# Kernel optimization log

Measured on AMD Instinct MI355X. Metric: run time of the kernel, lower is better.

## Reference

```python
import jax, jax.numpy as jnp
import numpy as np
from jax import lax

B, N, G, K, D = 16, 8192, 256, 64, 256
DEPTH, H, HID, PH = 4, 8, 1024, 128
EPS = 1e-5
BN_SCALE = float(1.0 / np.sqrt(1.0 + 1e-5))  # BatchNorm eval, running mean 0 / var 1


def setup_inputs() -> dict:
    key = jax.random.key(0)
    ks = iter(jax.random.split(key, 48))
    def rn(shape, s=0.02):
        return jax.random.normal(next(ks), shape, jnp.float32) * s
    z = lambda *s: jnp.zeros(s, jnp.float32)
    o = lambda *s: jnp.ones(s, jnp.float32)
    return dict(
        x=jax.random.normal(next(ks), (B, N, 3), jnp.float32),
        enc_w1=rn((3, 128)), enc_b1=z(128), enc_bn1_g=o(128), enc_bn1_b=z(128),
        enc_w2=rn((128, 256)), enc_b2=z(256),
        enc_w3=rn((512, 512)), enc_b3=z(512), enc_bn2_g=o(512), enc_bn2_b=z(512),
        enc_w4=rn((512, D)), enc_b4=z(D),
        cls_token=rn((1, 1, D)), cls_pos=rn((1, 1, D)),
        pos_w1=rn((3, 128)), pos_b1=z(128), pos_w2=rn((128, D)), pos_b2=z(D),
        ln1_g=o(DEPTH, D), ln1_b=z(DEPTH, D),
        qkv_w=rn((DEPTH, D, 3 * D)),
        proj_w=rn((DEPTH, D, D)), proj_b=z(DEPTH, D),
        ln2_g=o(DEPTH, D), ln2_b=z(DEPTH, D),
        fc1_w=rn((DEPTH, D, HID)), fc1_b=z(DEPTH, HID),
        fc2_w=rn((DEPTH, HID, D)), fc2_b=z(DEPTH, D),
        norm_g=o(D), norm_b=z(D),
        head_w1=rn((D + 3, PH)), head_b1=z(PH), head_w2=rn((PH, 1)), head_b2=z(1),
    )


def layernorm(t, g, b):
    m = jnp.mean(t, -1, keepdims=True)
    v = jnp.mean((t - m) ** 2, -1, keepdims=True)
    return (t - m) / jnp.sqrt(v + EPS) * g + b


def fps(xyz, num_group):
    # farthest point sampling; deterministic start at index 0 (torch uses randint)
    Bb, Nn, _ = xyz.shape
    def body(i, st):
        dist, far, idxs = st
        idxs = idxs.at[:, i].set(far)
        cen = jnp.take_along_axis(xyz, far[:, None, None], axis=1)  # (B,1,3)
        d = jnp.sum((xyz - cen) ** 2, -1)
        dist = jnp.minimum(dist, d)
        far = jnp.argmax(dist, axis=1).astype(jnp.int32)
        return (dist, far, idxs)
    st0 = (jnp.full((Bb, Nn), 1e10, jnp.float32),
           jnp.zeros((Bb,), jnp.int32),
           jnp.zeros((Bb, num_group), jnp.int32))
    _, _, idxs = lax.fori_loop(0, num_group, body, st0)
    centers = jnp.take_along_axis(xyz, idxs[..., None], axis=1)  # (B,G,3)
    return centers, idxs


def knn(xyz, centers, k):
    # squared-distance cdist (same argsort order as p=2) + topk smallest
    c2 = jnp.sum(centers ** 2, -1)[:, :, None]
    x2 = jnp.sum(xyz ** 2, -1)[:, None, :]
    d2 = c2 + x2 - 2.0 * jnp.einsum('bgd,bnd->bgn', centers, xyz)  # (B,G,N)
    idx = lax.top_k(-d2, k)[1]  # (B,G,k)
    neigh = jax.vmap(lambda p, i: p[i])(xyz, idx)  # (B,G,k,3)
    return idx, neigh


def _forward(x, enc_w1, enc_b1, enc_bn1_g, enc_bn1_b, enc_w2, enc_b2,
             enc_w3, enc_b3, enc_bn2_g, enc_bn2_b, enc_w4, enc_b4,
             cls_token, cls_pos, pos_w1, pos_b1, pos_w2, pos_b2,
             ln1_g, ln1_b, qkv_w, proj_w, proj_b, ln2_g, ln2_b,
             fc1_w, fc1_b, fc2_w, fc2_b, norm_g, norm_b,
             head_w1, head_b1, head_w2, head_b2):
    Bb, Nn, _ = x.shape
    # grouping is @torch.no_grad() in the original -> stop_gradient
    pts = lax.stop_gradient(x)
    centers, _ = fps(pts, G)
    idx, neigh = knn(pts, centers, K)
    neigh = neigh - centers[:, :, None, :]  # (B,G,K,3) centered

    # PointNet encoder (kernel-size-1 convs == matmuls; BN eval with unit stats)
    pg = neigh.reshape(Bb * G, K, 3)
    h = pg @ enc_w1 + enc_b1                                # (BG,K,128)
    h = jax.nn.relu(h * enc_bn1_g * BN_SCALE + enc_bn1_b)
    h = h @ enc_w2 + enc_b2                                 # (BG,K,256)
    gmax = jnp.max(h, axis=1, keepdims=True)                # (BG,1,256)
    h = jnp.concatenate([jnp.broadcast_to(gmax, h.shape), h], -1)  # (BG,K,512)
    h = h @ enc_w3 + enc_b3
    h = jax.nn.relu(h * enc_bn2_g * BN_SCALE + enc_bn2_b)
    h = h @ enc_w4 + enc_b4                                 # (BG,K,D)
    tokens = jnp.max(h, axis=1).reshape(Bb, G, D)

    pos = jax.nn.gelu(centers @ pos_w1 + pos_b1, approximate=False) @ pos_w2 + pos_b2
    xt = jnp.concatenate([jnp.broadcast_to(cls_token, (Bb, 1, D)), tokens], 1)
    pt = jnp.concatenate([jnp.broadcast_to(cls_pos, (Bb, 1, D)), pos], 1)

    scale = (D // H) ** -0.5
    for l in range(DEPTH):
        xi = xt + pt  # pos added before every block
        h1 = layernorm(xi, ln1_g[l], ln1_b[l])
        qkv = (h1 @ qkv_w[l]).reshape(Bb, G + 1, 3, H, D // H).transpose(2, 0, 3, 1, 4)
        q, k_, v = qkv[0], qkv[1], qkv[2]
        attn = jax.nn.softmax(jnp.einsum('bhnd,bhmd->bhnm', q, k_) * scale, -1)
        o = jnp.einsum('bhnm,bhmd->bhnd', attn, v).transpose(0, 2, 1, 3).reshape(Bb, G + 1, D)
        xi = xi + o @ proj_w[l] + proj_b[l]
        h2 = layernorm(xi, ln2_g[l], ln2_b[l])
        xi = xi + jax.nn.gelu(h2 @ fc1_w[l] + fc1_b[l], approximate=False) @ fc2_w[l] + fc2_b[l]
        xt = xi
    xt = layernorm(xt, norm_g, norm_b)

    gfeat = xt[:, 1:, :]  # (B,G,D)
    concat = jnp.concatenate(
        [jnp.broadcast_to(gfeat[:, :, None, :], (Bb, G, K, D)), neigh], -1)  # (B,G,K,D+3)
    lg = (jax.nn.relu(concat @ head_w1 + head_b1) @ head_w2 + head_b2)[..., 0]  # (B,G,K)

    # scatter-mean per-point logits over original N points
    flat_i = idx.reshape(Bb, G * K)
    flat_v = lg.reshape(Bb, G * K)
    sums = jax.vmap(lambda v, i: jax.ops.segment_sum(v, i, num_segments=N))(flat_v, flat_i)
    cnts = jax.vmap(lambda i: jax.ops.segment_sum(jnp.ones(i.shape, jnp.float32), i, num_segments=N))(flat_i)
    return sums / jnp.maximum(cnts, 1.0)  # (B,N)


def reference(x, enc_w1, enc_b1, enc_bn1_g, enc_bn1_b, enc_w2, enc_b2,
              enc_w3, enc_b3, enc_bn2_g, enc_bn2_b, enc_w4, enc_b4,
              cls_token, cls_pos, pos_w1, pos_b1, pos_w2, pos_b2,
              ln1_g, ln1_b, qkv_w, proj_w, proj_b, ln2_g, ln2_b,
              fc1_w, fc1_b, fc2_w, fc2_b, norm_g, norm_b,
              head_w1, head_b1, head_w2, head_b2):
    return _forward(x, enc_w1, enc_b1, enc_bn1_g, enc_bn1_b, enc_w2, enc_b2,
                    enc_w3, enc_b3, enc_bn2_g, enc_bn2_b, enc_w4, enc_b4,
                    cls_token, cls_pos, pos_w1, pos_b1, pos_w2, pos_b2,
                    ln1_g, ln1_b, qkv_w, proj_w, proj_b, ln2_g, ln2_b,
                    fc1_w, fc1_b, fc2_w, fc2_b, norm_g, norm_b,
                    head_w1, head_b1, head_w2, head_b2)
```

## Files before the change

kernel.cpp:

```cpp
#include <hip/hip_runtime.h>
#include <hip/hip_bf16.h>

#define B_ 16
#define N_ 8192
#define G_ 256
#define K_ 64
#define D_ 256
#define HID_ 1024
#define EPS_ 1e-5f

typedef __attribute__((ext_vector_type(8))) short bf16x8;
typedef __attribute__((ext_vector_type(4))) float f32x4;

__device__ __forceinline__ float bf16_to_f32(unsigned short u){
  unsigned int v = ((unsigned int)u) << 16;
  return __uint_as_float(v);
}
__device__ __forceinline__ unsigned short f32_to_bf16(float f){
  unsigned int u = __float_as_uint(f);
  unsigned int r = (u + 0x7FFFu + ((u >> 16) & 1u)) >> 16;
  return (unsigned short)r;
}
__device__ __forceinline__ unsigned short bf16h(float a){
  __hip_bfloat16 h = __float2bfloat16(a);
  union { __hip_bfloat16 h; unsigned short u; } cv; cv.h = h; return cv.u;
}
__device__ __forceinline__ float gelu_exact(float v){
  return 0.5f * v * (1.0f + erff(v * 0.70710678118654752440f));
}

template<int CTRL>
__device__ __forceinline__ unsigned long long dpp64(unsigned long long k){
  int lo = (int)(unsigned int)k;
  int hi = (int)(unsigned int)(k >> 32);
  int dlo = __builtin_amdgcn_update_dpp(lo, lo, CTRL, 0xF, 0xF, false);
  int dhi = __builtin_amdgcn_update_dpp(hi, hi, CTRL, 0xF, 0xF, false);
  return (((unsigned long long)(unsigned int)dhi) << 32) | (unsigned int)dlo;
}
__device__ __forceinline__ unsigned long long bcast64(unsigned long long k, int lane){
  unsigned int lo = (unsigned int)__builtin_amdgcn_readlane((int)(unsigned int)k, lane);
  unsigned int hi = (unsigned int)__builtin_amdgcn_readlane((int)(unsigned int)(k >> 32), lane);
  return (((unsigned long long)hi) << 32) | lo;
}
__device__ __forceinline__ unsigned long long wave_max64(unsigned long long k){
  unsigned long long t;
  t = dpp64<0x111>(k); if (t > k) k = t;
  t = dpp64<0x112>(k); if (t > k) k = t;
  t = dpp64<0x114>(k); if (t > k) k = t;
  t = dpp64<0x118>(k); if (t > k) k = t;
  t = dpp64<0x142>(k); if (t > k) k = t;
  t = dpp64<0x143>(k); if (t > k) k = t;
  return bcast64(k, 63);
}
__device__ __forceinline__ unsigned long long wave_min64(unsigned long long k){
  unsigned long long t;
  t = dpp64<0x111>(k); if (t < k) k = t;
  t = dpp64<0x112>(k); if (t < k) k = t;
  t = dpp64<0x114>(k); if (t < k) k = t;
  t = dpp64<0x118>(k); if (t < k) k = t;
  t = dpp64<0x142>(k); if (t < k) k = t;
  t = dpp64<0x143>(k); if (t < k) k = t;
  return bcast64(k, 63);
}
__device__ __forceinline__ unsigned long long red8_max64(unsigned long long k){
  unsigned long long t;
  t = dpp64<0x111>(k); if (t > k) k = t;
  t = dpp64<0x112>(k); if (t > k) k = t;
  t = dpp64<0x114>(k); if (t > k) k = t;
  return bcast64(k, 7);
}
__device__ __forceinline__ unsigned long long red4_min64(unsigned long long k){
  unsigned long long t;
  t = dpp64<0x111>(k); if (t < k) k = t;
  t = dpp64<0x112>(k); if (t < k) k = t;
  return bcast64(k, 3);
}

__device__ __forceinline__ void packHi(const float* __restrict__ W, unsigned short* __restrict__ hi,
                                       int f, int N, int ksBits){
  int j = f & 7, lane = (f >> 3) & 63;
  int ks = (f >> 9) & ((1 << ksBits) - 1);
  int nt = f >> (9 + ksBits);
  int k = ks * 32 + ((lane >> 4) & 3) * 8 + j, c = nt * 16 + (lane & 15);
  hi[f] = f32_to_bf16(W[(size_t)k * N + c]);
}

__global__ __launch_bounds__(512) void prep_fps_kernel(
    const float* __restrict__ x, float* __restrict__ centers,
    const float* __restrict__ w1, const float* __restrict__ b1,
    const float* __restrict__ g1, const float* __restrict__ bb1,
    const float* __restrict__ w3, const float* __restrict__ b3,
    const float* __restrict__ g2, const float* __restrict__ bb2,
    const float* __restrict__ enc_w2, const float* __restrict__ enc_w4,
    const float* __restrict__ qkv_w, const float* __restrict__ proj_w,
    const float* __restrict__ fc1_w, const float* __restrict__ fc2_w,
    float* __restrict__ w1f, float* __restrict__ b1f, float* __restrict__ b3f,
    unsigned short* __restrict__ w2ph, unsigned short* __restrict__ w2pl,
    unsigned short* __restrict__ w3ph, unsigned short* __restrict__ w4ph,
    unsigned short* __restrict__ qkvPh, unsigned short* __restrict__ projPh,
    unsigned short* __restrict__ fc1Ph, unsigned short* __restrict__ fc2Ph,
    unsigned short* __restrict__ w3tp)
{
  const float S = 0.99999500003749968f;
  int blk = blockIdx.x, tid = threadIdx.x;

  if (blk >= 17){
    int f = (blk - 17) * 512 + tid;
    if (f < 32768){
      int j = f & 7, lane = (f >> 3) & 63, ks = (f >> 9) & 3, nt = f >> 11;
      int k = ks * 32 + ((lane >> 4) & 3) * 8 + j, c = nt * 16 + (lane & 15);
      float v = enc_w2[(size_t)k * 256 + c];
      unsigned short h = f32_to_bf16(v);
      w2ph[f] = h; w2pl[f] = f32_to_bf16(v - bf16_to_f32(h));
    } else if (f < 163840){
      f -= 32768;
      int j = f & 7, lane = (f >> 3) & 63, ks = (f >> 9) & 7, nt = f >> 12;
      int k = ks * 32 + ((lane >> 4) & 3) * 8 + j, c = nt * 16 + (lane & 15);
      w3ph[f] = f32_to_bf16(w3[(size_t)(256 + k) * 512 + c] * g2[c] * S);
    } else if (f < 294912){
      f -= 163840;
      packHi(enc_w4, w4ph, f, 256, 4);
    } else if (f < 1081344){
      f -= 294912;
      int l = f / 196608, fl = f - l * 196608;
      packHi(qkv_w + (size_t)l * 196608, qkvPh + (size_t)l * 196608, fl, 768, 3);
    } else if (f < 1343488){
      f -= 1081344;
      int l = f >> 16, fl = f & 65535;
      packHi(proj_w + (size_t)l * 65536, projPh + (size_t)l * 65536, fl, 256, 3);
    } else if (f < 2392064){
      f -= 1343488;
      int l = f >> 18, fl = f & 262143;
      packHi(fc1_w + (size_t)l * 262144, fc1Ph + (size_t)l * 262144, fl, 1024, 3);
    } else if (f < 3440640){
      f -= 2392064;
      int l = f >> 18, fl = f & 262143;
      packHi(fc2_w + (size_t)l * 262144, fc2Ph + (size_t)l * 262144, fl, 256, 5);
    } else {
      f -= 3440640;
      int j = f & 7, lane = (f >> 3) & 63, ks = (f >> 9) & 7, nt = f >> 12;
      int k = ks * 32 + ((lane >> 4) & 3) * 8 + j, c = nt * 16 + (lane & 15);
      w3tp[f] = f32_to_bf16(w3[(size_t)k * 512 + c] * g2[c] * S);
    }
    return;
  }
  if (blk == 16){
    if (tid < 384) w1f[tid] = w1[tid] * g1[tid & 127] * S;
    if (tid < 128) b1f[tid] = b1[tid] * g1[tid] * S + bb1[tid];
    b3f[tid] = b3[tid] * g2[tid] * S + bb2[tid];
    return;
  }

  int b = blk;
  const float* xb = x + (size_t)b * N_ * 3;
  int lane = tid & 63, wave = tid >> 6;
  float px[16], py[16], pz[16], dist[16];
#pragma unroll
  for (int j = 0; j < 16; j++){
    int p = tid + j * 512;
    px[j] = xb[p*3+0]; py[j] = xb[p*3+1]; pz[j] = xb[p*3+2];
    dist[j] = 1e10f;
  }
  __shared__ unsigned long long slotK[2][8];
  __shared__ float4 slotC[2][8];
  __shared__ float sCen[G_ * 3];
  float cx = xb[0], cy = xb[1], cz = xb[2];
  for (int i = 0; i < G_; i++){
    if (tid == 0){
      sCen[i*3+0] = cx; sCen[i*3+1] = cy; sCen[i*3+2] = cz;
    }
    float bestv = -1.0f; int bestj = 0;
#pragma unroll
    for (int j = 0; j < 16; j++){
      float dx = __fadd_rn(px[j], -cx);
      float dy = __fadd_rn(py[j], -cy);
      float dz = __fadd_rn(pz[j], -cz);
      float d  = __fadd_rn(__fadd_rn(__fmul_rn(dx,dx), __fmul_rn(dy,dy)), __fmul_rn(dz,dz));
      float dm = fminf(dist[j], d);
      dist[j] = dm;
      if (dm > bestv){ bestv = dm; bestj = j; }
    }
    unsigned int pid = (unsigned int)(tid + bestj * 512);
    unsigned long long key = (((unsigned long long)__float_as_uint(bestv)) << 32) | (unsigned long long)(~pid);
    key = wave_max64(key);
    int par = i & 1;
    unsigned int wpid = ~(unsigned int)key;
    if (lane == (int)(wpid & 63)){
      int jj = (int)(wpid >> 9);
      float fx = px[0], fy = py[0], fz = pz[0];
#pragma unroll
      for (int j = 1; j < 16; j++) if (jj == j){ fx = px[j]; fy = py[j]; fz = pz[j]; }
      slotK[par][wave] = key;
      slotC[par][wave] = make_float4(fx, fy, fz, 0.0f);
    }
    __syncthreads();
    if (i + 1 < G_){
      int sl = lane & 7;
      unsigned long long k2 = slotK[par][sl];
      float4 cc4 = slotC[par][sl];
      k2 = red8_max64(k2);
      unsigned int gpid = ~(unsigned int)k2;
      int s = (int)((gpid & 511u) >> 6);
      cx = __uint_as_float((unsigned int)__builtin_amdgcn_readlane((int)__float_as_uint(cc4.x), s));
      cy = __uint_as_float((unsigned int)__builtin_amdgcn_readlane((int)__float_as_uint(cc4.y), s));
      cz = __uint_as_float((unsigned int)__builtin_amdgcn_readlane((int)__float_as_uint(cc4.z), s));
    }
  }
  __syncthreads();
  for (int e = tid; e < G_ * 3; e += 512)
    centers[(size_t)b * G_ * 3 + e] = sCen[e];
}

__global__ __launch_bounds__(256) void knn_kernel(const float* __restrict__ x, const float* __restrict__ centers,
                                                  int* __restrict__ knn_idx, float* __restrict__ neigh)
{
  int blk = blockIdx.x, b = blk >> 8;
  const float* xb = x + (size_t)b * N_ * 3;
  const float* cc = centers + (size_t)blk * 3;
  int tid = threadIdx.x, lane = tid & 63, wave = tid >> 6;
  float c0 = cc[0], c1 = cc[1], c2v = cc[2];
  float c2s = __fadd_rn(__fadd_rn(__fmul_rn(c0,c0), __fmul_rn(c1,c1)), __fmul_rn(c2v,c2v));
  float d[32];
#pragma unroll
  for (int j = 0; j < 32; j++){
    int p = tid + j * 256;
    float x0 = xb[p*3+0], x1 = xb[p*3+1], x2 = xb[p*3+2];
    float xs = __fadd_rn(__fadd_rn(__fmul_rn(x0,x0), __fmul_rn(x1,x1)), __fmul_rn(x2,x2));
    float dt = __fadd_rn(__fadd_rn(__fmul_rn(c0,x0), __fmul_rn(c1,x1)), __fmul_rn(c2v,x2));
    d[j] = __fadd_rn(__fadd_rn(c2s, xs), -__fmul_rn(2.0f, dt));
  }
  const float FINF = __int_as_float(0x7F800000);
  float lmin = FINF; unsigned int lp = 0xFFFFFFFFu;
#pragma unroll
  for (int j = 0; j < 32; j++){ if (d[j] < lmin){ lmin = d[j]; lp = (unsigned int)(tid + j*256); } }
  __shared__ unsigned long long wred[2][4];
  __shared__ int sIdx[K_];
  __shared__ float sNei[K_ * 3];
  for (int r = 0; r < K_; r++){
    unsigned int u = __float_as_uint(lmin);
    u = (u & 0x80000000u) ? ~u : (u | 0x80000000u);
    unsigned long long key = (((unsigned long long)u) << 32) | (unsigned long long)lp;
    key = wave_min64(key);
    int cur = r & 1;
    if (lane == 0) wred[cur][wave] = key;
    __syncthreads();
    unsigned long long m = red4_min64(wred[cur][lane & 3]);
    unsigned int p = (unsigned int)(m & 0xFFFFFFFFull);
    if (tid == (p & 255u)){
      sIdx[r] = (int)p;
      sNei[r*3+0] = __fadd_rn(xb[p*3+0], -c0);
      sNei[r*3+1] = __fadd_rn(xb[p*3+1], -c1);
      sNei[r*3+2] = __fadd_rn(xb[p*3+2], -c2v);
      lmin = FINF; lp = 0xFFFFFFFFu;
#pragma unroll
      for (int j = 0; j < 32; j++){
        if ((unsigned int)(tid + j*256) == p) d[j] = FINF;
        if (d[j] < lmin){ lmin = d[j]; lp = (unsigned int)(tid + j*256); }
      }
    }
  }
  __syncthreads();
  if (tid < K_) knn_idx[(size_t)blk * K_ + tid] = sIdx[tid];
  if (tid < K_ * 3) neigh[(size_t)blk * K_ * 3 + tid] = sNei[tid];
}

__global__ __launch_bounds__(256, 2) void encoder_kernel(
    const float* __restrict__ neigh,
    const float* __restrict__ w1f, const float* __restrict__ b1f,
    const unsigned short* __restrict__ w2ph, const unsigned short* __restrict__ w2pl,
    const float* __restrict__ b2,
    const float* __restrict__ b3f,
    const unsigned short* __restrict__ w3ph, const unsigned short* __restrict__ w3tp,
    const unsigned short* __restrict__ w4ph,
    const float* __restrict__ b4,
    float* __restrict__ tokens)
{
  __shared__ __align__(16) unsigned short sH1[64 * 136];
  __shared__ __align__(16) unsigned short sH2[64 * 264];
  __shared__ __align__(16) float sShared[256];
  float (*sNeigh)[4] = (float(*)[4])sShared;
  unsigned short* sGmaxBf = (unsigned short*)sShared;

  int tid  = threadIdx.x;
  int wave = tid >> 6, lane = tid & 63, quad = lane >> 4, lrow = lane & 15;
  size_t gid = blockIdx.x;

  if (tid < 192) sNeigh[tid / 3][tid % 3] = neigh[gid * 192 + tid];
  __syncthreads();

  for (int e = tid; e < 8192; e += 256){
    int r = e >> 7, c = e & 127;
    float v = fmaf(sNeigh[r][2], w1f[256 + c], fmaf(sNeigh[r][1], w1f[128 + c], fmaf(sNeigh[r][0], w1f[c], b1f[c])));
    sH1[r * 136 + c] = bf16h(fmaxf(v, 0.0f));
  }
  __syncthreads();

  {
    f32x4 acc[4][4];
    const f32x4 z = {0.f, 0.f, 0.f, 0.f};
#pragma unroll
    for (int mt = 0; mt < 4; mt++)
#pragma unroll
      for (int nl = 0; nl < 4; nl++) acc[mt][nl] = z;
#pragma unroll
    for (int ks = 0; ks < 4; ks++){
      bf16x8 af[4];
#pragma unroll
      for (int mt = 0; mt < 4; mt++)
        af[mt] = *(const bf16x8*)&sH1[(mt*16 + lrow)*136 + ks*32 + quad*8];
#pragma unroll
      for (int nl = 0; nl < 4; nl++){
        size_t bo = (((size_t)(wave*4 + nl)*4 + ks)*64 + lane)*8;
        bf16x8 bh = *(const bf16x8*)&w2ph[bo];
        bf16x8 bl = *(const bf16x8*)&w2pl[bo];
#pragma unroll
        for (int mt = 0; mt < 4; mt++){
          acc[mt][nl] = __builtin_amdgcn_mfma_f32_16x16x32_bf16(af[mt], bh, acc[mt][nl], 0, 0, 0);
          acc[mt][nl] = __builtin_amdgcn_mfma_f32_16x16x32_bf16(af[mt], bl, acc[mt][nl], 0, 0, 0);
        }
      }
    }
#pragma unroll
    for (int nl = 0; nl < 4; nl++){
      int col = wave*64 + nl*16 + lrow;
      float bias = b2[col];
#pragma unroll
      for (int mt = 0; mt < 4; mt++)
#pragma unroll
        for (int rg = 0; rg < 4; rg++)
          sH2[(mt*16 + quad*4 + rg)*264 + col] = bf16h(acc[mt][nl][rg] + bias);
    }
  }
  __syncthreads();

  {
    float mx = -3.4e38f;
#pragma unroll 8
    for (int r = 0; r < 64; r++) mx = fmaxf(mx, bf16_to_f32(sH2[r*264 + tid]));
    sGmaxBf[tid] = bf16h(mx);
  }
  __syncthreads();

  f32x4 acc4[4][4];
  {
    const f32x4 z = {0.f, 0.f, 0.f, 0.f};
#pragma unroll
    for (int mt = 0; mt < 4; mt++)
#pragma unroll
      for (int nl = 0; nl < 4; nl++) acc4[mt][nl] = z;
  }
  for (int cc = 0; cc < 4; cc++){
    f32x4 acc3[4][2], accg[2];
    {
      const f32x4 z = {0.f, 0.f, 0.f, 0.f};
#pragma unroll
      for (int mt = 0; mt < 4; mt++){ acc3[mt][0] = z; acc3[mt][1] = z; }
      accg[0] = z; accg[1] = z;
    }
#pragma unroll
    for (int ks = 0; ks < 8; ks++){
      bf16x8 gf = *(const bf16x8*)&sGmaxBf[ks*32 + quad*8];
#pragma unroll
      for (int nl = 0; nl < 2; nl++){
        int nt = cc*8 + wave*2 + nl;
        size_t bo = (((size_t)nt*8 + ks)*64 + lane)*8;
        bf16x8 bh = *(const bf16x8*)&w3tp[bo];
        accg[nl] = __builtin_amdgcn_mfma_f32_16x16x32_bf16(gf, bh, accg[nl], 0, 0, 0);
      }
    }
#pragma unroll
    for (int ks = 0; ks < 8; ks++){
      bf16x8 af[4];
#pragma unroll
      for (int mt = 0; mt < 4; mt++)
        af[mt] = *(const bf16x8*)&sH2[(mt*16 + lrow)*264 + ks*32 + quad*8];
#pragma unroll
      for (int nl = 0; nl < 2; nl++){
        int nt = cc*8 + wave*2 + nl;
        size_t bo = (((size_t)nt*8 + ks)*64 + lane)*8;
        bf16x8 bh = *(const bf16x8*)&w3ph[bo];
#pragma unroll
        for (int mt = 0; mt < 4; mt++)
          acc3[mt][nl] = __builtin_amdgcn_mfma_f32_16x16x32_bf16(af[mt], bh, acc3[mt][nl], 0, 0, 0);
      }
    }
    __syncthreads();
#pragma unroll
    for (int nl = 0; nl < 2; nl++){
      int cl = wave*32 + nl*16 + lrow;
      int c  = cc*128 + cl;
      float bb = b3f[c];
#pragma unroll
      for (int mt = 0; mt < 4; mt++)
#pragma unroll
        for (int rg = 0; rg < 4; rg++)
          sH1[(mt*16 + quad*4 + rg)*136 + cl] = bf16h(fmaxf(acc3[mt][nl][rg] + accg[nl][rg] + bb, 0.0f));
    }
    __syncthreads();
#pragma unroll
    for (int ks = 0; ks < 4; ks++){
      bf16x8 af[4];
#pragma unroll
      for (int mt = 0; mt < 4; mt++)
        af[mt] = *(const bf16x8*)&sH1[(mt*16 + lrow)*136 + ks*32 + quad*8];
#pragma unroll
      for (int nl = 0; nl < 4; nl++){
        int nt = wave*4 + nl;
        size_t bo = (((size_t)nt*16 + cc*4 + ks)*64 + lane)*8;
        bf16x8 bh = *(const bf16x8*)&w4ph[bo];
#pragma unroll
        for (int mt = 0; mt < 4; mt++)
          acc4[mt][nl] = __builtin_amdgcn_mfma_f32_16x16x32_bf16(af[mt], bh, acc4[mt][nl], 0, 0, 0);
      }
    }
  }

#pragma unroll
  for (int nl = 0; nl < 4; nl++){
    float mx = -3.4e38f;
#pragma unroll
    for (int mt = 0; mt < 4; mt++)
#pragma unroll
      for (int rg = 0; rg < 4; rg++) mx = fmaxf(mx, acc4[mt][nl][rg]);
    mx = fmaxf(mx, __shfl_xor(mx, 16));
    mx = fmaxf(mx, __shfl_xor(mx, 32));
    if (quad == 0){
      int col = wave*64 + nl*16 + lrow;
      tokens[gid * 256 + col] = mx + b4[col];
    }
  }
}

__global__ __launch_bounds__(128) void pos_ln_kernel(
    const float* __restrict__ centers, const float* __restrict__ tokens,
    const float* __restrict__ cls_token, const float* __restrict__ cls_pos,
    const float* __restrict__ pw1, const float* __restrict__ pb1,
    const float* __restrict__ pw2, const float* __restrict__ pb2,
    const float* __restrict__ lng, const float* __restrict__ lnb,
    float* __restrict__ pt, float* __restrict__ xi, unsigned short* __restrict__ lnbuf)
{
  __shared__ float hS[128];
  __shared__ float red[2][2];
  int row = blockIdx.x;
  int b = row / 257, n = row - b * 257;
  int tid = threadIdx.x;
  size_t ro = (size_t)row * 256;
  float u0, u1;
  if (n == 0){
    float p0 = cls_pos[tid], p1 = cls_pos[128 + tid];
    u0 = cls_token[tid] + p0; u1 = cls_token[128 + tid] + p1;
    pt[ro + tid] = p0; pt[ro + 128 + tid] = p1;
  } else {
    int g = n - 1;
    const float* c = centers + ((size_t)b * 256 + g) * 3;
    float h = fmaf(c[2], pw1[256 + tid], fmaf(c[1], pw1[128 + tid], fmaf(c[0], pw1[tid], pb1[tid])));
    hS[tid] = gelu_exact(h);
    __syncthreads();
    const float* tok = tokens + ((size_t)b * 256 + g) * 256;
    float s0 = pb2[tid], s1 = pb2[128 + tid];
#pragma unroll 4
    for (int k = 0; k < 128; k++){
      s0 = fmaf(hS[k], pw2[(size_t)k * 256 + tid], s0);
      s1 = fmaf(hS[k], pw2[(size_t)k * 256 + 128 + tid], s1);
    }
    pt[ro + tid] = s0; pt[ro + 128 + tid] = s1;
    u0 = tok[tid] + s0; u1 = tok[128 + tid] + s1;
  }
  float s = u0 + u1, q = u0*u0 + u1*u1;
#pragma unroll
  for (int o = 32; o; o >>= 1){ s += __shfl_down(s, o); q += __shfl_down(q, o); }
  int wv = tid >> 6;
  if ((tid & 63) == 0){ red[0][wv] = s; red[1][wv] = q; }
  __syncthreads();
  float m  = (red[0][0] + red[0][1]) * (1.0f / 256.0f);
  float var = (red[1][0] + red[1][1]) * (1.0f / 256.0f) - m * m;
  float rs = 1.0f / sqrtf(var + EPS_);
  xi[ro + tid] = u0; xi[ro + 128 + tid] = u1;
  lnbuf[ro + tid] = bf16h((u0 - m) * rs * lng[tid] + lnb[tid]);
  lnbuf[ro + 128 + tid] = bf16h((u1 - m) * rs * lng[128 + tid] + lnb[128 + tid]);
}

template<int ACT>
__global__ __launch_bounds__(256) void mfma_gemm(
    const unsigned short* __restrict__ A, const unsigned short* __restrict__ Bh,
    const float* __restrict__ bias, unsigned short* __restrict__ C, int M, int K, int N)
{
  __shared__ __align__(16) unsigned short sA[32 * 72];
  int tid = threadIdx.x;
  int wave = tid >> 6, lane = tid & 63, quad = lane >> 4, lrow = lane & 15;
  int row0 = blockIdx.x * 32;
  int col0 = blockIdx.y * 128;
  int ksTotal = K >> 5;
  f32x4 acc[2][2];
  const f32x4 z = {0.f, 0.f, 0.f, 0.f};
#pragma unroll
  for (int mt = 0; mt < 2; mt++){ acc[mt][0] = z; acc[mt][1] = z; }

  for (int k0 = 0; k0 < K; k0 += 64){
    {
      int r = tid >> 3, c8 = (tid & 7) * 8;
      int gr = row0 + r;
      bf16x8 v = {0,0,0,0,0,0,0,0};
      if (gr < M) v = *(const bf16x8*)(A + (size_t)gr * K + k0 + c8);
      *(bf16x8*)&sA[r * 72 + c8] = v;
    }
    __syncthreads();
    int ksBase = k0 >> 5;
#pragma unroll
    for (int ks = 0; ks < 2; ks++){
      bf16x8 af[2];
#pragma unroll
      for (int mt = 0; mt < 2; mt++)
        af[mt] = *(const bf16x8*)&sA[(mt*16 + lrow)*72 + ks*32 + quad*8];
#pragma unroll
      for (int nl = 0; nl < 2; nl++){
        int nt = (col0 >> 4) + wave*2 + nl;
        size_t bo = (((size_t)nt * ksTotal + ksBase + ks)*64 + lane)*8;
        bf16x8 bh = *(const bf16x8*)&Bh[bo];
#pragma unroll
        for (int mt = 0; mt < 2; mt++)
          acc[mt][nl] = __builtin_amdgcn_mfma_f32_16x16x32_bf16(af[mt], bh, acc[mt][nl], 0, 0, 0);
      }
    }
    __syncthreads();
  }
#pragma unroll
  for (int nl = 0; nl < 2; nl++){
    int c = col0 + wave*32 + nl*16 + lrow;
    float bc = bias ? bias[c] : 0.0f;
#pragma unroll
    for (int mt = 0; mt < 2; mt++)
#pragma unroll
      for (int rg = 0; rg < 4; rg++){
        int r = row0 + mt*16 + quad*4 + rg;
        if (r < M){
          float v = acc[mt][nl][rg] + bc;
          if (ACT == 1) v = gelu_exact(v);
          C[(size_t)r * N + c] = bf16h(v);
        }
      }
  }
}

__global__ __launch_bounds__(256) void mfma_gemm_ln(
    const unsigned short* __restrict__ A, const unsigned short* __restrict__ Bh,
    const float* __restrict__ bias, const float* __restrict__ res,
    const float* __restrict__ ptb,
    float* __restrict__ C, float* __restrict__ xiOut, unsigned short* __restrict__ lnOut,
    const float* __restrict__ lng, const float* __restrict__ lnb, int M, int K)
{
  __shared__ __align__(16) unsigned short sA[16 * 72];
  __shared__ float sRed[2][16][4];
  int tid = threadIdx.x;
  int wave = tid >> 6, lane = tid & 63, quad = lane >> 4, lrow = lane & 15;
  int row0 = blockIdx.x * 16;
  int ksTotal = K >> 5;
  f32x4 acc[4];
  const f32x4 z = {0.f, 0.f, 0.f, 0.f};
#pragma unroll
  for (int nl = 0; nl < 4; nl++) acc[nl] = z;

  for (int k0 = 0; k0 < K; k0 += 64){
    if (tid < 128){
      int r = tid >> 3, c8 = (tid & 7) * 8;
      int gr = row0 + r;
      bf16x8 v = {0,0,0,0,0,0,0,0};
      if (gr < M) v = *(const bf16x8*)(A + (size_t)gr * K + k0 + c8);
      *(bf16x8*)&sA[r * 72 + c8] = v;
    }
    __syncthreads();
    int ksBase = k0 >> 5;
#pragma unroll
    for (int ks = 0; ks < 2; ks++){
      bf16x8 af = *(const bf16x8*)&sA[lrow*72 + ks*32 + quad*8];
#pragma unroll
      for (int nl = 0; nl < 4; nl++){
        int nt = wave*4 + nl;
        size_t bo = (((size_t)nt * ksTotal + ksBase + ks)*64 + lane)*8;
        bf16x8 bh = *(const bf16x8*)&Bh[bo];
        acc[nl] = __builtin_amdgcn_mfma_f32_16x16x32_bf16(af, bh, acc[nl], 0, 0, 0);
      }
    }
    __syncthreads();
  }
#pragma unroll
  for (int nl = 0; nl < 4; nl++){
    int c = wave*64 + nl*16 + lrow;
    float bc = bias[c];
#pragma unroll
    for (int rg = 0; rg < 4; rg++){
      int r = row0 + quad*4 + rg;
      if (r < M){
        float v = acc[nl][rg] + bc + res[(size_t)r * 256 + c];
        if (C) C[(size_t)r * 256 + c] = v;
        float u = v;
        if (ptb) u += ptb[(size_t)r * 256 + c];
        acc[nl][rg] = u;
      }
    }
  }
#pragma unroll
  for (int rg = 0; rg < 4; rg++){
    int rloc = quad*4 + rg;
    float s = 0.0f, q = 0.0f;
#pragma unroll
    for (int nl = 0; nl < 4; nl++){ float u = acc[nl][rg]; s += u; q += u*u; }
#pragma unroll
    for (int off = 1; off < 16; off <<= 1){ s += __shfl_xor(s, off); q += __shfl_xor(q, off); }
    if (lrow == 0){ sRed[0][rloc][wave] = s; sRed[1][rloc][wave] = q; }
  }
  __syncthreads();
#pragma unroll
  for (int rg = 0; rg < 4; rg++){
    int rloc = quad*4 + rg;
    int r = row0 + rloc;
    if (r >= M) continue;
    float s = ((sRed[0][rloc][0] + sRed[0][rloc][1]) + sRed[0][rloc][2]) + sRed[0][rloc][3];
    float q = ((sRed[1][rloc][0] + sRed[1][rloc][1]) + sRed[1][rloc][2]) + sRed[1][rloc][3];
    float m  = s * (1.0f / 256.0f);
    float var = q * (1.0f / 256.0f) - m * m;
    float rs = 1.0f / sqrtf(var + EPS_);
#pragma unroll
    for (int nl = 0; nl < 4; nl++){
      int c = wave*64 + nl*16 + lrow;
      float u = acc[nl][rg];
      lnOut[(size_t)r * 256 + c] = bf16h((u - m) * rs * lng[c] + lnb[c]);
      if (xiOut) xiOut[(size_t)r * 256 + c] = u;
    }
  }
}

__global__ __launch_bounds__(256) void attn_kernel(const unsigned short* __restrict__ qkv, unsigned short* __restrict__ obuf)
{
  int bh = blockIdx.x;
  int b = bh >> 3, h = bh & 7;
  int tid = threadIdx.x;
  int qi = tid >> 2, kp = tid & 3;
  int qrow = blockIdx.y * 64 + qi;
  bool act = qrow < 257;
  __shared__ float kS[128][33];
  __shared__ float vS[128][33];
  const unsigned short* qb = qkv + (size_t)b * 257 * 768;
  float q[32], o[32];
  float mrun = -3.4e38f, l = 0.0f;
  if (act){
    const unsigned short* qr = qb + (size_t)qrow * 768 + h * 32;
#pragma unroll
    for (int j = 0; j < 32; j++){ q[j] = bf16_to_f32(qr[j]); o[j] = 0.0f; }
  }
  const float scale = 0.17677669529663687f;
  for (int m0 = 0; m0 < 257; m0 += 128){
    int cnt = min(128, 257 - m0);
    for (int e = tid; e < cnt * 32; e += 256){
      int mm = e >> 5, j = e & 31;
      const unsigned short* rowp = qb + (size_t)(m0 + mm) * 768 + h * 32;
      kS[mm][j] = bf16_to_f32(rowp[256 + j]);
      vS[mm][j] = bf16_to_f32(rowp[512 + j]);
    }
    __syncthreads();
    if (act){
      for (int mm = kp; mm < cnt; mm += 4){
        float s = 0.0f;
#pragma unroll
        for (int j = 0; j < 32; j++) s = fmaf(q[j], kS[mm][j], s);
        s *= scale;
        float nm = fmaxf(mrun, s);
        float alpha = expf(mrun - nm);
        float p = expf(s - nm);
        l = fmaf(l, alpha, p);
#pragma unroll
        for (int j = 0; j < 32; j++) o[j] = fmaf(p, vS[mm][j], o[j] * alpha);
        mrun = nm;
      }
    }
    __syncthreads();
  }
  if (act){
#pragma unroll
    for (int msk = 1; msk <= 2; msk <<= 1){
      float m2 = __shfl_xor(mrun, msk);
      float l2 = __shfl_xor(l, msk);
      float nm = fmaxf(mrun, m2);
      float a1 = expf(mrun - nm), a2 = expf(m2 - nm);
      l = l * a1 + l2 * a2;
#pragma unroll
      for (int j = 0; j < 32; j++){
        float o2 = __shfl_xor(o[j], msk);
        o[j] = o[j] * a1 + o2 * a2;
      }
      mrun = nm;
    }
    if (kp == 0){
      float inv = 1.0f / l;
      unsigned short* orow = obuf + (size_t)(b * 257 + qrow) * 256 + h * 32;
#pragma unroll
      for (int j = 0; j < 32; j++) orow[j] = bf16h(o[j] * inv);
    }
  }
}

__global__ __launch_bounds__(256) void head_kernel(
    const unsigned short* __restrict__ gfeat, const float* __restrict__ neigh, const int* __restrict__ knn_idx,
    const float* __restrict__ w1, const float* __restrict__ b1,
    const float* __restrict__ w2, const float* __restrict__ b2,
    float* __restrict__ sums, float* __restrict__ cnts)
{
  int blk = blockIdx.x, b = blk >> 8;
  __shared__ float xS[256];
  __shared__ float nS[64][4];
  __shared__ float partH[2][128];
  __shared__ float sharedH[128];
  __shared__ float w2S[128];
  __shared__ float wtail[3][128];
  int tid = threadIdx.x;
  xS[tid] = bf16_to_f32(gfeat[((size_t)b * 257 + 1 + (blk & 255)) * 256 + tid]);
  if (tid < 192) nS[tid / 3][tid % 3] = neigh[(size_t)blk * 192 + tid];
  if (tid < 128){
    w2S[tid] = w2[tid];
    wtail[0][tid] = w1[256 * 128 + tid];
    wtail[1][tid] = w1[257 * 128 + tid];
    wtail[2][tid] = w1[258 * 128 + tid];
  }
  __syncthreads();
  {
    int half = tid >> 7, j = tid & 127;
    float s = 0.0f;
#pragma unroll 8
    for (int k = 0; k < 128; k++) s = fmaf(xS[half * 128 + k], w1[(size_t)(half * 128 + k) * 128 + j], s);
    partH[half][j] = s;
  }
  __syncthreads();
  if (tid < 128) sharedH[tid] = partH[0][tid] + partH[1][tid] + b1[tid];
  __syncthreads();
  int r = tid >> 2, q = tid & 3;
  float n0 = nS[r][0], n1 = nS[r][1], n2 = nS[r][2];
  float s = 0.0f;
#pragma unroll
  for (int j0 = 0; j0 < 32; j0++){
    int j = q * 32 + j0;
    float h = fmaf(n2, wtail[2][j], fmaf(n1, wtail[1][j], fmaf(n0, wtail[0][j], sharedH[j])));
    s = fmaf(fmaxf(h, 0.0f), w2S[j], s);
  }
  s += __shfl_xor(s, 1);
  s += __shfl_xor(s, 2);
  if (q == 0){
    float lg = s + b2[0];
    int p = knn_idx[(size_t)blk * K_ + r];
    atomicAdd(&sums[(size_t)b * N_ + p], lg);
    atomicAdd(&cnts[(size_t)b * N_ + p], 1.0f);
  }
}

__global__ void finalize_kernel(const float* __restrict__ sums, const float* __restrict__ cnts, float* __restrict__ out)
{
  int i = blockIdx.x * 256 + threadIdx.x;
  out[i] = sums[i] / fmaxf(cnts[i], 1.0f);
}

extern "C" void kernel_launch(void* const* d_in, const int* in_sizes, int n_in,
                              void* d_out, int out_size, void* d_ws, size_t ws_size,
                              hipStream_t stream)
{
  (void)in_sizes; (void)n_in; (void)out_size; (void)ws_size;
  const float* x        = (const float*)d_in[0];
  const float* enc_w1   = (const float*)d_in[1];
  const float* enc_b1   = (const float*)d_in[2];
  const float* enc_bn1g = (const float*)d_in[3];
  const float* enc_bn1b = (const float*)d_in[4];
  const float* enc_w2   = (const float*)d_in[5];
  const float* enc_b2   = (const float*)d_in[6];
  const float* enc_w3   = (const float*)d_in[7];
  const float* enc_b3   = (const float*)d_in[8];
  const float* enc_bn2g = (const float*)d_in[9];
  const float* enc_bn2b = (const float*)d_in[10];
  const float* enc_w4   = (const float*)d_in[11];
  const float* enc_b4   = (const float*)d_in[12];
  const float* cls_tok  = (const float*)d_in[13];
  const float* cls_pos  = (const float*)d_in[14];
  const float* pos_w1   = (const float*)d_in[15];
  const float* pos_b1   = (const float*)d_in[16];
  const float* pos_w2   = (const float*)d_in[17];
  const float* pos_b2   = (const float*)d_in[18];
  const float* ln1_g    = (const float*)d_in[19];
  const float* ln1_b    = (const float*)d_in[20];
  const float* qkv_w    = (const float*)d_in[21];
  const float* proj_w   = (const float*)d_in[22];
  const float* proj_b   = (const float*)d_in[23];
  const float* ln2_g    = (const float*)d_in[24];
  const float* ln2_b    = (const float*)d_in[25];
  const float* fc1_w    = (const float*)d_in[26];
  const float* fc1_b    = (const float*)d_in[27];
  const float* fc2_w    = (const float*)d_in[28];
  const float* fc2_b    = (const float*)d_in[29];
  const float* norm_g   = (const float*)d_in[30];
  const float* norm_b   = (const float*)d_in[31];
  const float* head_w1  = (const float*)d_in[32];
  const float* head_b1  = (const float*)d_in[33];
  const float* head_w2  = (const float*)d_in[34];
  const float* head_b2  = (const float*)d_in[35];

  float* ws = (float*)d_ws;
  size_t off = 0;
  auto alloc = [&](size_t n)->float*{ float* p = ws + off; off += (n + 63) & ~(size_t)63; return p; };

  float* centers = alloc((size_t)B_ * G_ * 3);
  float* w1f     = alloc(384);
  float* b1f     = alloc(128);
  float* b3f     = alloc(512);
  unsigned short* w2ph = (unsigned short*)alloc(16384);
  unsigned short* w2pl = (unsigned short*)alloc(16384);
  unsigned short* w3ph = (unsigned short*)alloc(65536);
  unsigned short* w3tp = (unsigned short*)alloc(65536);
  unsigned short* w4ph = (unsigned short*)alloc(65536);
  unsigned short* qkvPh = (unsigned short*)alloc(393216);
  unsigned short* projPh = (unsigned short*)alloc(131072);
  unsigned short* fc1Ph = (unsigned short*)alloc(524288);
  unsigned short* fc2Ph = (unsigned short*)alloc(524288);
  float* tokens  = alloc((size_t)B_ * G_ * D_);
  float* neigh   = alloc((size_t)B_ * G_ * K_ * 3);
  int*   knn_idx = (int*)alloc((size_t)B_ * G_ * K_);
  float* pt      = alloc((size_t)B_ * 257 * D_);
  float* xi      = alloc((size_t)B_ * 257 * D_);
  unsigned short* lnbufB = (unsigned short*)alloc((size_t)B_ * 257 * D_ / 2 + 64);
  unsigned short* obufB  = (unsigned short*)alloc((size_t)B_ * 257 * D_ / 2 + 64);
  unsigned short* bigbufB= (unsigned short*)alloc((size_t)B_ * 257 * HID_ / 2 + 64);
  unsigned short* gfeatB = (unsigned short*)alloc((size_t)B_ * 257 * D_ / 2 + 64);
  float* sums    = alloc((size_t)B_ * N_);
  float* cnts    = alloc((size_t)B_ * N_);

  hipMemsetAsync(sums, 0, (size_t)2 * B_ * N_ * sizeof(float), stream);

  prep_fps_kernel<<<6993, 512, 0, stream>>>(x, centers,
      enc_w1, enc_b1, enc_bn1g, enc_bn1b, enc_w3, enc_b3, enc_bn2g, enc_bn2b,
      enc_w2, enc_w4, qkv_w, proj_w, fc1_w, fc2_w,
      w1f, b1f, b3f, w2ph, w2pl, w3ph, w4ph, qkvPh, projPh, fc1Ph, fc2Ph, w3tp);

  knn_kernel<<<B_ * G_, 256, 0, stream>>>(x, centers, knn_idx, neigh);
  encoder_kernel<<<B_ * G_, 256, 0, stream>>>(neigh, w1f, b1f, w2ph, w2pl, enc_b2,
                                              b3f, w3ph, w3tp, w4ph, enc_b4, tokens);
  pos_ln_kernel<<<B_ * 257, 128, 0, stream>>>(centers, tokens, cls_tok, cls_pos,
                                              pos_w1, pos_b1, pos_w2, pos_b2,
                                              ln1_g, ln1_b, pt, xi, lnbufB);
  const int M = B_ * 257;
  for (int l = 0; l < 4; l++){
    mfma_gemm<0><<<dim3(129, 6), 256, 0, stream>>>(lnbufB, qkvPh + (size_t)l*196608, nullptr, bigbufB, M, 256, 768);
    attn_kernel<<<dim3(B_ * 8, 5), 256, 0, stream>>>(bigbufB, obufB);
    mfma_gemm_ln<<<257, 256, 0, stream>>>(obufB, projPh + (size_t)l*65536, proj_b + l*256, xi, nullptr,
                                          xi, nullptr, lnbufB, ln2_g + l*256, ln2_b + l*256, M, 256);
    mfma_gemm<1><<<dim3(129, 8), 256, 0, stream>>>(lnbufB, fc1Ph + (size_t)l*262144, fc1_b + l*1024, bigbufB, M, 256, 1024);
    if (l < 3){
      mfma_gemm_ln<<<257, 256, 0, stream>>>(bigbufB, fc2Ph + (size_t)l*262144, fc2_b + l*256, xi, pt,
                                            nullptr, xi, lnbufB, ln1_g + (l+1)*256, ln1_b + (l+1)*256, M, 1024);
    } else {
      mfma_gemm_ln<<<257, 256, 0, stream>>>(bigbufB, fc2Ph + (size_t)l*262144, fc2_b + l*256, xi, nullptr,
                                            nullptr, nullptr, gfeatB, norm_g, norm_b, M, 1024);
    }
  }
  head_kernel<<<B_ * G_, 256, 0, stream>>>(gfeatB, neigh, knn_idx, head_w1, head_b1, head_w2, head_b2, sums, cnts);
  finalize_kernel<<<(B_ * N_) / 256, 256, 0, stream>>>(sums, cnts, (float*)d_out);
}
```

Measured before the change: 1.650 ms.

## Fuse transformer MLP fc1+GELU+fc2+LayerNorm into one kernel; add occupancy hints

Adds an mlp_fused kernel that computes fc1 with GELU into a 16x1024 shared-memory hidden tile, then runs fc2, the residual add and LayerNorm in the same block. This drops the fc1 GEMM launch and the round trip of the 4112x1024 bf16 hidden activation through global memory. Each block now reads the full fc1 weight matrix from global or L2 with no tiling reuse across blocks, and uses 16 accumulator tiles per wave, which may raise register pressure. Separately, min-blocks-per-CU hints are added to several kernels' launch bounds.

```diff
diff --git a/kernel.cpp b/kernel.cpp
--- a/kernel.cpp
+++ b/kernel.cpp
@@ -85,7 +85,7 @@
   hi[f] = f32_to_bf16(W[(size_t)k * N + c]);
 }
 
-__global__ __launch_bounds__(512) void prep_fps_kernel(
+__global__ __launch_bounds__(512, 2) void prep_fps_kernel(
     const float* __restrict__ x, float* __restrict__ centers,
     const float* __restrict__ w1, const float* __restrict__ b1,
     const float* __restrict__ g1, const float* __restrict__ bb1,
@@ -211,8 +211,8 @@
     centers[(size_t)b * G_ * 3 + e] = sCen[e];
 }
 
-__global__ __launch_bounds__(256) void knn_kernel(const float* __restrict__ x, const float* __restrict__ centers,
-                                                  int* __restrict__ knn_idx, float* __restrict__ neigh)
+__global__ __launch_bounds__(256, 4) void knn_kernel(const float* __restrict__ x, const float* __restrict__ centers,
+                                                     int* __restrict__ knn_idx, float* __restrict__ neigh)
 {
   int blk = blockIdx.x, b = blk >> 8;
   const float* xb = x + (size_t)b * N_ * 3;
@@ -481,7 +481,7 @@
 }
 
 template<int ACT>
-__global__ __launch_bounds__(256) void mfma_gemm(
+__global__ __launch_bounds__(256, 2) void mfma_gemm(
     const unsigned short* __restrict__ A, const unsigned short* __restrict__ Bh,
     const float* __restrict__ bias, unsigned short* __restrict__ C, int M, int K, int N)
 {
@@ -542,7 +542,7 @@
   }
 }
 
-__global__ __launch_bounds__(256) void mfma_gemm_ln(
+__global__ __launch_bounds__(256, 2) void mfma_gemm_ln(
     const unsigned short* __restrict__ A, const unsigned short* __restrict__ Bh,
     const float* __restrict__ bias, const float* __restrict__ res,
     const float* __restrict__ ptb,
@@ -630,7 +630,122 @@
   }
 }
 
-__global__ __launch_bounds__(256) void attn_kernel(const unsigned short* __restrict__ qkv, unsigned short* __restrict__ obuf)
+__global__ __launch_bounds__(256, 2) void mlp_fused(
+    const unsigned short* __restrict__ A,
+    const unsigned short* __restrict__ B1,
+    const float* __restrict__ bias1,
+    const unsigned short* __restrict__ B2,
+    const float* __restrict__ bias2,
+    const float* __restrict__ res,
+    const float* __restrict__ ptb,
+    float* __restrict__ xiOut, unsigned short* __restrict__ lnOut,
+    const float* __restrict__ lng, const float* __restrict__ lnb, int M)
+{
+  __shared__ __align__(16) unsigned short sA[16 * 264];
+  __shared__ __align__(16) unsigned short sH[16 * 1032];
+  __shared__ float sRed[2][16][4];
+  int tid = threadIdx.x;
+  int wave = tid >> 6, lane = tid & 63, quad = lane >> 4, lrow = lane & 15;
+  int row0 = blockIdx.x * 16;
+
+  for (int e = tid; e < 512; e += 256){
+    int r = e >> 5, c8 = (e & 31) * 8;
+    int gr = row0 + r;
+    bf16x8 v = {0,0,0,0,0,0,0,0};
+    if (gr < M) v = *(const bf16x8*)(A + (size_t)gr * 256 + c8);
+    *(bf16x8*)&sA[r * 264 + c8] = v;
+  }
+  __syncthreads();
+
+  {
+    f32x4 acc1[16];
+    const f32x4 z = {0.f, 0.f, 0.f, 0.f};
+#pragma unroll
+    for (int nl = 0; nl < 16; nl++) acc1[nl] = z;
+#pragma unroll
+    for (int ks = 0; ks < 8; ks++){
+      bf16x8 af = *(const bf16x8*)&sA[lrow*264 + ks*32 + quad*8];
+#pragma unroll
+      for (int nl = 0; nl < 16; nl++){
+        int nt = wave*16 + nl;
+        size_t bo = (((size_t)nt*8 + ks)*64 + lane)*8;
+        bf16x8 bh = *(const bf16x8*)&B1[bo];
+        acc1[nl] = __builtin_amdgcn_mfma_f32_16x16x32_bf16(af, bh, acc1[nl], 0, 0, 0);
+      }
+    }
+#pragma unroll
+    for (int nl = 0; nl < 16; nl++){
+      int c = wave*256 + nl*16 + lrow;
+      float bc = bias1[c];
+#pragma unroll
+      for (int rg = 0; rg < 4; rg++)
+        sH[(quad*4+rg)*1032 + c] = bf16h(gelu_exact(acc1[nl][rg] + bc));
+    }
+  }
+  __syncthreads();
+
+  f32x4 acc[4];
+  const f32x4 z = {0.f, 0.f, 0.f, 0.f};
+#pragma unroll
+  for (int nl = 0; nl < 4; nl++) acc[nl] = z;
+#pragma unroll 4
+  for (int ks = 0; ks < 32; ks++){
+    bf16x8 af = *(const bf16x8*)&sH[lrow*1032 + ks*32 + quad*8];
+#pragma unroll
+    for (int nl = 0; nl < 4; nl++){
+      int nt = wave*4 + nl;
+      size_t bo = (((size_t)nt*32 + ks)*64 + lane)*8;
+      bf16x8 bh = *(const bf16x8*)&B2[bo];
+      acc[nl] = __builtin_amdgcn_mfma_f32_16x16x32_bf16(af, bh, acc[nl], 0, 0, 0);
+    }
+  }
+#pragma unroll
+  for (int nl = 0; nl < 4; nl++){
+    int c = wave*64 + nl*16 + lrow;
+    float bc = bias2[c];
+#pragma unroll
+    for (int rg = 0; rg < 4; rg++){
+      int r = row0 + quad*4 + rg;
+      if (r < M){
+        float v = acc[nl][rg] + bc + res[(size_t)r * 256 + c];
+        float u = v;
+        if (ptb) u += ptb[(size_t)r * 256 + c];
+        acc[nl][rg] = u;
+      }
+    }
+  }
+#pragma unroll
+  for (int rg = 0; rg < 4; rg++){
+    int rloc = quad*4 + rg;
+    float s = 0.0f, q = 0.0f;
+#pragma unroll
+    for (int nl = 0; nl < 4; nl++){ float u = acc[nl][rg]; s += u; q += u*u; }
+#pragma unroll
+    for (int off = 1; off < 16; off <<= 1){ s += __shfl_xor(s, off); q += __shfl_xor(q, off); }
+    if (lrow == 0){ sRed[0][rloc][wave] = s; sRed[1][rloc][wave] = q; }
+  }
+  __syncthreads();
+#pragma unroll
+  for (int rg = 0; rg < 4; rg++){
+    int rloc = quad*4 + rg;
+    int r = row0 + rloc;
+    if (r >= M) continue;
+    float s = ((sRed[0][rloc][0] + sRed[0][rloc][1]) + sRed[0][rloc][2]) + sRed[0][rloc][3];
+    float q = ((sRed[1][rloc][0] + sRed[1][rloc][1]) + sRed[1][rloc][2]) + sRed[1][rloc][3];
+    float m  = s * (1.0f / 256.0f);
+    float var = q * (1.0f / 256.0f) - m * m;
+    float rs = 1.0f / sqrtf(var + EPS_);
+#pragma unroll
+    for (int nl = 0; nl < 4; nl++){
+      int c = wave*64 + nl*16 + lrow;
+      float u = acc[nl][rg];
+      lnOut[(size_t)r * 256 + c] = bf16h((u - m) * rs * lng[c] + lnb[c]);
+      if (xiOut) xiOut[(size_t)r * 256 + c] = u;
+    }
+  }
+}
+
+__global__ __launch_bounds__(256, 2) void attn_kernel(const unsigned short* __restrict__ qkv, unsigned short* __restrict__ obuf)
 {
   int bh = blockIdx.x;
   int b = bh >> 3, h = bh & 7;
@@ -847,13 +962,14 @@
     attn_kernel<<<dim3(B_ * 8, 5), 256, 0, stream>>>(bigbufB, obufB);
     mfma_gemm_ln<<<257, 256, 0, stream>>>(obufB, projPh + (size_t)l*65536, proj_b + l*256, xi, nullptr,
                                           xi, nullptr, lnbufB, ln2_g + l*256, ln2_b + l*256, M, 256);
-    mfma_gemm<1><<<dim3(129, 8), 256, 0, stream>>>(lnbufB, fc1Ph + (size_t)l*262144, fc1_b + l*1024, bigbufB, M, 256, 1024);
     if (l < 3){
-      mfma_gemm_ln<<<257, 256, 0, stream>>>(bigbufB, fc2Ph + (size_t)l*262144, fc2_b + l*256, xi, pt,
-                                            nullptr, xi, lnbufB, ln1_g + (l+1)*256, ln1_b + (l+1)*256, M, 1024);
+      mlp_fused<<<257, 256, 0, stream>>>(lnbufB, fc1Ph + (size_t)l*262144, fc1_b + l*1024,
+                                         fc2Ph + (size_t)l*262144, fc2_b + l*256, xi, pt,
+                                         xi, lnbufB, ln1_g + (l+1)*256, ln1_b + (l+1)*256, M);
     } else {
-      mfma_gemm_ln<<<257, 256, 0, stream>>>(bigbufB, fc2Ph + (size_t)l*262144, fc2_b + l*256, xi, nullptr,
-                                            nullptr, nullptr, gfeatB, norm_g, norm_b, M, 1024);
+      mlp_fused<<<257, 256, 0, stream>>>(lnbufB, fc1Ph + (size_t)l*262144, fc1_b + l*1024,
+                                         fc2Ph + (size_t)l*262144, fc2_b + l*256, xi, nullptr,
+                                         nullptr, gfeatB, norm_g, norm_b, M);
     }
   }
   head_kernel<<<B_ * G_, 256, 0, stream>>>(gfeatB, neigh, knn_idx, head_w1, head_b1, head_w2, head_b2, sums, cnts);
```

New measurement: 1.584 ms. -4.0%, faster.
